# Performance work log

Hardware: AMD Instinct MI355X
Metric: run time of the kernel (lower is better)

## Reference

```python
import jax, jax.numpy as jnp
import numpy as np

HIDDEN = 1024
HEADS = 16
HEAD_DIM = HIDDEN // HEADS
B, S = 2, 2048


def setup_inputs() -> dict:
    key = jax.random.key(0)
    k1, k2, k3 = jax.random.split(key, 3)
    scale_in = 1.0 / np.sqrt(HIDDEN)
    x = jax.random.normal(k1, (B, S, HIDDEN), dtype=jnp.float32)
    wqkv_w = jax.random.normal(k2, (3 * HIDDEN, HIDDEN), dtype=jnp.float32) * scale_in
    wo_w = jax.random.normal(k3, (HIDDEN, HIDDEN), dtype=jnp.float32) * scale_in
    wo_b = jnp.zeros((HIDDEN,), dtype=jnp.float32)
    return {"x": x, "wqkv_w": wqkv_w, "wo_w": wo_w, "wo_b": wo_b}


def reference(x, wqkv_w, wo_w, wo_b):
    b, s, d = x.shape
    h, hd = HEADS, HEAD_DIM
    sm_scale = hd ** (-0.5)
    # QKV projection (torch Linear: x @ W^T), then chunk into q,k,v
    qkv = jnp.einsum('bsd,ed->bse', x, wqkv_w)  # [b, s, 3d]
    q, k, v = jnp.split(qkv, 3, axis=-1)
    # [b, h, s, hd]
    q = q.reshape(b, s, h, hd).transpose(0, 2, 1, 3)
    k = k.reshape(b, s, h, hd).transpose(0, 2, 1, 3)
    v = v.reshape(b, s, h, hd).transpose(0, 2, 1, 3)
    # raw scores, then causal mask (mask applied BEFORE scaling, as in source;
    # -inf * scale == -inf so math matches softmax(score*scale) with mask)
    scores = jnp.einsum('bhqe,bhke->bhqk', q, k)
    causal = jnp.tril(jnp.ones((s, s), dtype=bool))
    scores = jnp.where(causal[None, None, :, :], scores, -jnp.inf)
    weights = jax.nn.softmax(scores * sm_scale, axis=-1)
    # dropout p=0.0 (eval) -> identity
    out = jnp.einsum('bhqk,bhke->bhqe', weights, v)
    out = out.transpose(0, 2, 1, 3).reshape(b, s, h * hd)
    y = jnp.einsum('bsd,ed->bse', out, wo_w) + wo_b
    return (y, k, v)
```

## Files before the change

kernel.cpp:

```cpp
#include <hip/hip_runtime.h>
#include <cstdint>
#include <cstddef>


using bf16x8 = __attribute__((ext_vector_type(8))) __bf16;
using f32x4  = __attribute__((ext_vector_type(4))) float;
using u16    = unsigned short;

#define SOFT_SCALE 0.1803368801111244f

__device__ __forceinline__ u16 f2bf(float f) {
  union { float f; uint32_t u; } a; a.f = f;
  uint32_t r = a.u + 0x7fffu + ((a.u >> 16) & 1u);
  return (u16)(r >> 16);
}

__device__ __forceinline__ bf16x8 ldfrag(const u16* p) {
  return *reinterpret_cast<const bf16x8*>(p);
}

__device__ __forceinline__ void gload_lds16(const void* g, void* l) {
  __builtin_amdgcn_global_load_lds((const __attribute__((address_space(1))) void*)g,
                                   (__attribute__((address_space(3))) void*)l,
                                   16, 0, 0);
}

__device__ __forceinline__ uint32_t cvt_pk_bf16(float a, float b) {
  uint32_t r;
  asm("v_cvt_pk_bf16_f32 %0, %1, %2" : "=v"(r) : "v"(a), "v"(b));
  return r;
}

__global__ void cvt_all(const float* __restrict__ x, const float* __restrict__ wqkv,
                        const float* __restrict__ wo,
                        u16* __restrict__ xb, u16* __restrict__ wqkvb, u16* __restrict__ wob) {
  int i = blockIdx.x * blockDim.x + threadIdx.x;
  int stride = gridDim.x * blockDim.x;
  for (; i < 2097152; i += stride) {
    const float* src; u16* dst; int j;
    if (i < 1048576)      { src = x;    dst = xb;    j = i; }
    else if (i < 1835008) { src = wqkv; dst = wqkvb; j = i - 1048576; }
    else                  { src = wo;   dst = wob;   j = i - 1835008; }
    float4 v = reinterpret_cast<const float4*>(src)[j];
    ushort4 o;
    o.x = f2bf(v.x); o.y = f2bf(v.y); o.z = f2bf(v.z); o.w = f2bf(v.w);
    reinterpret_cast<ushort4*>(dst)[j] = o;
  }
}

__global__ __launch_bounds__(512, 2) void qkv_gemm_kernel(
    const u16* __restrict__ Xb, const u16* __restrict__ Wb,
    u16* __restrict__ Qws, u16* __restrict__ Kws, u16* __restrict__ Vtws,
    float* __restrict__ out) {
  extern __shared__ char smem[];

  const int tid = threadIdx.x, lane = tid & 63, wid = tid >> 6;
  const int wr = wid >> 2, wc = wid & 3;
  const int fq = lane >> 4, fr = lane & 15;

  const int wg = (blockIdx.x & 7) * 24 + (blockIdx.x >> 3);
  const int bm = wg / 12, bn = wg % 12;
  const int m0 = bm * 256, n0 = bn * 256;

  const char* Ab = (const char*)Xb + (size_t)m0 * 2048;
  const char* Bb = (const char*)Wb + (size_t)n0 * 2048;

  f32x4 acc[8][4] = {};

  auto stage = [&](int t, int cc) {
    char* As = smem + cc * 32768;
    char* Bs = smem + 65536 + cc * 32768;
#pragma unroll
    for (int f = 0; f < 4; ++f) {
      int lin = (f * 512 + tid) * 16;
      int row = lin >> 7;
      int col = (lin & 127) ^ ((row & 7) << 4);
      gload_lds16(Ab + (size_t)row * 2048 + t * 128 + col, As + lin);
      gload_lds16(Bb + (size_t)row * 2048 + t * 128 + col, Bs + lin);
    }
  };

  stage(0, 0);
  int cur = 0;
  for (int t = 0; t < 16; ++t) {
    if (t < 15) {
      stage(t + 1, cur ^ 1);
      asm volatile("s_waitcnt vmcnt(8)" ::: "memory");
    } else {
      asm volatile("s_waitcnt vmcnt(0)" ::: "memory");
    }
    __builtin_amdgcn_s_barrier();
    __builtin_amdgcn_sched_barrier(0);

    const char* As = smem + cur * 32768;
    const char* Bs = smem + 65536 + cur * 32768;

#pragma unroll
    for (int ks = 0; ks < 2; ++ks) {
      bf16x8 af[8];
#pragma unroll
      for (int m = 0; m < 8; ++m) {
        int row = wr * 128 + m * 16 + fr;
        int col = (ks * 64 + fq * 16) ^ ((row & 7) << 4);
        af[m] = *(const bf16x8*)(As + row * 128 + col);
      }
#pragma unroll
      for (int nh = 0; nh < 2; ++nh) {
        int row0 = wc * 64 + (nh * 2) * 16 + fr;
        int col0 = (ks * 64 + fq * 16) ^ ((row0 & 7) << 4);
        bf16x8 bf0 = *(const bf16x8*)(Bs + row0 * 128 + col0);
        int row1 = wc * 64 + (nh * 2 + 1) * 16 + fr;
        int col1 = (ks * 64 + fq * 16) ^ ((row1 & 7) << 4);
        bf16x8 bf1 = *(const bf16x8*)(Bs + row1 * 128 + col1);
        __builtin_amdgcn_s_setprio(1);
#pragma unroll
        for (int m = 0; m < 8; ++m) {
          acc[m][nh * 2]     = __builtin_amdgcn_mfma_f32_16x16x32_bf16(af[m], bf0, acc[m][nh * 2], 0, 0, 0);
          acc[m][nh * 2 + 1] = __builtin_amdgcn_mfma_f32_16x16x32_bf16(af[m], bf1, acc[m][nh * 2 + 1], 0, 0, 0);
        }
        __builtin_amdgcn_s_setprio(0);
      }
    }
    asm volatile("s_waitcnt lgkmcnt(0)" ::: "memory");
    __builtin_amdgcn_s_barrier();
    cur ^= 1;
  }

  const int sect = n0 >> 10;
  const int nn0 = (n0 & 1023) + wc * 64;
  const int mbase = m0 + wr * 128;
#pragma unroll
  for (int m = 0; m < 8; ++m)
#pragma unroll
    for (int n = 0; n < 4; ++n) {
      int mB = mbase + m * 16 + fq * 4;
      int ncol = nn0 + n * 16 + fr;
      int b = mB >> 11, s0 = mB & 2047;
      int h = ncol >> 6, hd = ncol & 63;
      size_t base = (((size_t)b * 16 + h) * 2048 + s0) * 64 + hd;
      float v0 = acc[m][n][0], v1 = acc[m][n][1], v2 = acc[m][n][2], v3 = acc[m][n][3];
      if (sect == 0) {
        Qws[base]       = f2bf(v0 * SOFT_SCALE);
        Qws[base + 64]  = f2bf(v1 * SOFT_SCALE);
        Qws[base + 128] = f2bf(v2 * SOFT_SCALE);
        Qws[base + 192] = f2bf(v3 * SOFT_SCALE);
      } else if (sect == 1) {
        Kws[base] = f2bf(v0); Kws[base + 64] = f2bf(v1);
        Kws[base + 128] = f2bf(v2); Kws[base + 192] = f2bf(v3);
        out[4194304 + base] = v0; out[4194304 + base + 64] = v1;
        out[4194304 + base + 128] = v2; out[4194304 + base + 192] = v3;
      } else {
        out[8388608 + base] = v0; out[8388608 + base + 64] = v1;
        out[8388608 + base + 128] = v2; out[8388608 + base + 192] = v3;
        size_t tt = ((size_t)(b * 16 + h) * 64 + hd) * 2048 + s0;
        ushort4 pk; pk.x = f2bf(v0); pk.y = f2bf(v1); pk.z = f2bf(v2); pk.w = f2bf(v3);
        *reinterpret_cast<ushort4*>(Vtws + tt) = pk;
      }
    }
}

__device__ __forceinline__ void gemm128_core(const u16* __restrict__ A,
                                             const u16* __restrict__ B,
                                             int m0, int n0, int K,
                                             u16* As, u16* Bs, f32x4 acc[4][4]) {
  const int tid  = threadIdx.x;
  const int lane = tid & 63;
  const int wid  = tid >> 6;
  const int wr = wid >> 1, wc = wid & 1;
  const int fq = lane >> 4, fr = lane & 15;

  for (int kb = 0; kb < K; kb += 32) {
#pragma unroll
    for (int j = 0; j < 2; ++j) {
      int lin = (j * 256 + tid) * 16;
      int row = lin >> 6;
      int rb  = lin & 63;
      gload_lds16((const char*)(A + (size_t)(m0 + row) * K + kb) + rb, (char*)As + lin);
      gload_lds16((const char*)(B + (size_t)(n0 + row) * K + kb) + rb, (char*)Bs + lin);
    }
    __syncthreads();

    bf16x8 av[4], bv[4];
#pragma unroll
    for (int i = 0; i < 4; ++i) av[i] = ldfrag(As + (wr * 64 + i * 16 + fr) * 32 + fq * 8);
#pragma unroll
    for (int j = 0; j < 4; ++j) bv[j] = ldfrag(Bs + (wc * 64 + j * 16 + fr) * 32 + fq * 8);
    __builtin_amdgcn_s_setprio(1);
#pragma unroll
    for (int i = 0; i < 4; ++i)
#pragma unroll
      for (int j = 0; j < 4; ++j)
        acc[i][j] = __builtin_amdgcn_mfma_f32_16x16x32_bf16(av[i], bv[j], acc[i][j], 0, 0, 0);
    __builtin_amdgcn_s_setprio(0);
    __syncthreads();
  }
}

__global__ __launch_bounds__(256, 4) void attn_kernel(
    const u16* __restrict__ Qw, const u16* __restrict__ Kw,
    const u16* __restrict__ Vtw, u16* __restrict__ Ow) {
  __shared__ u16 Ks[2][64 * 64];
  __shared__ u16 Vs[2][64 * 64];

  const int tid = threadIdx.x, lane = tid & 63, wid = tid >> 6;
  const int fq = lane >> 4, fr = lane & 15;
  const int bh = blockIdx.x & 31;
  const int qb = 31 - (blockIdx.x >> 5);
  const int b = bh >> 4, h = bh & 15;
  const int q0 = qb * 64;

  const u16* Qbase  = Qw  + (size_t)bh * 2048 * 64;
  const u16* Kbase  = Kw  + (size_t)bh * 2048 * 64;
  const char* VtBase = (const char*)(Vtw + (size_t)bh * 64 * 2048);

#pragma unroll
  for (int f = 0; f < 2; ++f) {
    int lin = (f * 256 + tid) * 16;
    int row = lin >> 7;
    int logical = lin ^ ((row & 7) << 4);
    gload_lds16((const char*)Kbase + logical, (char*)Ks[0] + lin);
    gload_lds16(VtBase + (size_t)row * 4096 + (logical & 127), (char*)Vs[0] + lin);
  }

  const int qrow = q0 + wid * 16 + fr;
  bf16x8 qa0 = ldfrag(Qbase + (size_t)qrow * 64 + fq * 8);
  bf16x8 qa1 = ldfrag(Qbase + (size_t)qrow * 64 + 32 + fq * 8);

  float ssum = 0.f;
  f32x4 accO[4] = {};

  int cur = 0;
  for (int kb = 0; kb <= qb; ++kb) {
    __syncthreads();

    if (kb < qb) {
      const char* kg = (const char*)(Kbase + (size_t)(kb + 1) * 64 * 64);
#pragma unroll
      for (int f = 0; f < 2; ++f) {
        int lin = (f * 256 + tid) * 16;
        int row = lin >> 7;
        int logical = lin ^ ((row & 7) << 4);
        gload_lds16(kg + logical, (char*)Ks[cur ^ 1] + lin);
        gload_lds16(VtBase + (size_t)row * 4096 + (size_t)(kb + 1) * 128 + (logical & 127),
                    (char*)Vs[cur ^ 1] + lin);
      }
    }

    const u16* Kc = Ks[cur];
    const u16* Vc = Vs[cur];

    f32x4 sfr[4];
    __builtin_amdgcn_s_setprio(1);
#pragma unroll
    for (int n = 0; n < 4; ++n) {
      int krow = n * 16 + fr;
      bf16x8 kf0 = ldfrag(Kc + krow * 64 + ((fq * 8)      ^ ((krow & 7) << 3)));
      bf16x8 kf1 = ldfrag(Kc + krow * 64 + ((fq * 8 + 32) ^ ((krow & 7) << 3)));
      f32x4 z = {};
      z = __builtin_amdgcn_mfma_f32_16x16x32_bf16(kf0, qa0, z, 0, 0, 0);
      z = __builtin_amdgcn_mfma_f32_16x16x32_bf16(kf1, qa1, z, 0, 0, 0);
      sfr[n] = z;
    }
    __builtin_amdgcn_s_setprio(0);

    uint32_t W[4][2];
#pragma unroll
    for (int n = 0; n < 4; ++n) {
      float p0, p1, p2, p3;
      if (kb < qb) {
        p0 = exp2f(sfr[n][0]);
        p1 = exp2f(sfr[n][1]);
        p2 = exp2f(sfr[n][2]);
        p3 = exp2f(sfr[n][3]);
      } else {
        int kvg = kb * 64 + n * 16 + fq * 4;
        p0 = (kvg + 0 > qrow) ? 0.f : exp2f(sfr[n][0]);
        p1 = (kvg + 1 > qrow) ? 0.f : exp2f(sfr[n][1]);
        p2 = (kvg + 2 > qrow) ? 0.f : exp2f(sfr[n][2]);
        p3 = (kvg + 3 > qrow) ? 0.f : exp2f(sfr[n][3]);
      }
      ssum += (p0 + p1) + (p2 + p3);
      W[n][0] = cvt_pk_bf16(p0, p1);
      W[n][1] = cvt_pk_bf16(p2, p3);
    }

    union { uint32_t u[4]; bf16x8 v; } pa0u, pa1u;
#pragma unroll
    for (int hh = 0; hh < 2; ++hh) {
      uint32_t a0 = W[0][hh], b0 = W[1][hh];
      asm("v_permlane32_swap_b32 %0, %1" : "+v"(a0), "+v"(b0));
      asm("v_permlane16_swap_b32 %0, %1" : "+v"(a0), "+v"(b0));
      pa0u.u[hh] = a0; pa0u.u[2 + hh] = b0;
      uint32_t a1 = W[2][hh], b1 = W[3][hh];
      asm("v_permlane32_swap_b32 %0, %1" : "+v"(a1), "+v"(b1));
      asm("v_permlane16_swap_b32 %0, %1" : "+v"(a1), "+v"(b1));
      pa1u.u[hh] = a1; pa1u.u[2 + hh] = b1;
    }

    __builtin_amdgcn_s_setprio(1);
#pragma unroll
    for (int nh = 0; nh < 4; ++nh) {
      int vrow = nh * 16 + fr;
      bf16x8 vb0 = ldfrag(Vc + vrow * 64 + ((fq * 8)      ^ ((vrow & 7) << 3)));
      bf16x8 vb1 = ldfrag(Vc + vrow * 64 + ((fq * 8 + 32) ^ ((vrow & 7) << 3)));
      accO[nh] = __builtin_amdgcn_mfma_f32_16x16x32_bf16(pa0u.v, vb0, accO[nh], 0, 0, 0);
      accO[nh] = __builtin_amdgcn_mfma_f32_16x16x32_bf16(pa1u.v, vb1, accO[nh], 0, 0, 0);
    }
    __builtin_amdgcn_s_setprio(0);
    cur ^= 1;
  }

  ssum += __shfl_xor(ssum, 16);
  ssum += __shfl_xor(ssum, 32);
  float inv = 1.0f / ssum;
  float invq[4];
#pragma unroll
  for (int r = 0; r < 4; ++r) invq[r] = __shfl(inv, fq * 4 + r);

#pragma unroll
  for (int nh = 0; nh < 4; ++nh)
#pragma unroll
    for (int r = 0; r < 4; ++r) {
      float o = accO[nh][r] * invq[r];
      int qr = q0 + wid * 16 + fq * 4 + r;
      Ow[((size_t)b * 2048 + qr) * 1024 + h * 64 + nh * 16 + fr] = f2bf(o);
    }
}

__global__ __launch_bounds__(256) void proj_gemm_kernel(
    const u16* __restrict__ Ob, const u16* __restrict__ Wob,
    const float* __restrict__ bias, float* __restrict__ out) {
  __shared__ u16 As[128 * 32];
  __shared__ u16 Bs[128 * 32];
  const int NB = 8;
  int m0 = (blockIdx.x / NB) * 128, n0 = (blockIdx.x % NB) * 128;
  f32x4 acc[4][4] = {};
  gemm128_core(Ob, Wob, m0, n0, 1024, As, Bs, acc);

  const int lane = threadIdx.x & 63, wid = threadIdx.x >> 6;
  const int wr = wid >> 1, wc = wid & 1, fq = lane >> 4, fr = lane & 15;
#pragma unroll
  for (int i = 0; i < 4; ++i)
#pragma unroll
    for (int j = 0; j < 4; ++j)
#pragma unroll
      for (int r = 0; r < 4; ++r) {
        int m = m0 + wr * 64 + i * 16 + fq * 4 + r;
        int n = n0 + wc * 64 + j * 16 + fr;
        out[(size_t)m * 1024 + n] = acc[i][j][r] + bias[n];
      }
}

extern "C" void kernel_launch(void* const* d_in, const int* in_sizes, int n_in,
                              void* d_out, int out_size, void* d_ws, size_t ws_size,
                              hipStream_t stream) {
  const float* x    = (const float*)d_in[0];
  const float* wqkv = (const float*)d_in[1];
  const float* wo   = (const float*)d_in[2];
  const float* wo_b = (const float*)d_in[3];
  float* out = (float*)d_out;

  u16* xb    = (u16*)d_ws;
  u16* wqkvb = xb    + 4194304;
  u16* wob   = wqkvb + 3145728;
  u16* q_ws  = wob   + 1048576;
  u16* k_ws  = q_ws  + 4194304;
  u16* vt_ws = k_ws  + 4194304;
  u16* o_ws  = vt_ws + 4194304;

  static bool attr_set = false;
  if (!attr_set) {
    hipFuncSetAttribute((const void*)qkv_gemm_kernel,
                        hipFuncAttributeMaxDynamicSharedMemorySize, 131072);
    attr_set = true;
  }

  cvt_all<<<2048, 256, 0, stream>>>(x, wqkv, wo, xb, wqkvb, wob);
  qkv_gemm_kernel<<<192, 512, 131072, stream>>>(xb, wqkvb, q_ws, k_ws, vt_ws, out);
  attn_kernel<<<32 * 32, 256, 0, stream>>>(q_ws, k_ws, vt_ws, o_ws);
  proj_gemm_kernel<<<32 * 8, 256, 0, stream>>>(o_ws, wob, wo_b, out);
}
```

Baseline: 119.1 us.

## Split long causal attention rows across two blocks and add a combine kernel

Query blocks in the upper half of the causal range now split their key range into two halves, each handled by its own block. Each half writes unnormalized bf16 partial outputs and row sums into reused workspace, and a new combine kernel adds them and normalizes. This shortens the critical path set by the longest causal rows and balances work across CUs. The cost is an extra kernel launch, extra partial-result traffic, and bf16 rounding of unnormalized partial sums.

```diff
diff --git a/kernel.cpp b/kernel.cpp
--- a/kernel.cpp
+++ b/kernel.cpp
@@ -13,6 +13,11 @@
   union { float f; uint32_t u; } a; a.f = f;
   uint32_t r = a.u + 0x7fffu + ((a.u >> 16) & 1u);
   return (u16)(r >> 16);
+}
+
+__device__ __forceinline__ float bf2f(u16 u) {
+  union { uint32_t u; float f; } a; a.u = ((uint32_t)u) << 16;
+  return a.f;
 }
 
 __device__ __forceinline__ bf16x8 ldfrag(const u16* p) {
@@ -198,14 +203,21 @@
 
 __global__ __launch_bounds__(256, 4) void attn_kernel(
     const u16* __restrict__ Qw, const u16* __restrict__ Kw,
-    const u16* __restrict__ Vtw, u16* __restrict__ Ow) {
+    const u16* __restrict__ Vtw, u16* __restrict__ Ow,
+    u16* __restrict__ Pb, float* __restrict__ Sb) {
   __shared__ u16 Ks[2][64 * 64];
   __shared__ u16 Vs[2][64 * 64];
 
   const int tid = threadIdx.x, lane = tid & 63, wid = tid >> 6;
   const int fq = lane >> 4, fr = lane & 15;
   const int bh = blockIdx.x & 31;
-  const int qb = 31 - (blockIdx.x >> 5);
+  const int j  = blockIdx.x >> 5;
+  int qb, sp, nsplit;
+  if (j < 32) { qb = 31 - (j >> 1); sp = j & 1; nsplit = 2; }
+  else        { qb = 47 - j;        sp = 0;     nsplit = 1; }
+  const int len = (qb + 2) >> 1;
+  const int lo  = (nsplit == 2) ? sp * len : 0;
+  const int hi  = (nsplit == 2) ? min(lo + len, qb + 1) : qb + 1;
   const int b = bh >> 4, h = bh & 15;
   const int q0 = qb * 64;
 
@@ -213,14 +225,19 @@
   const u16* Kbase  = Kw  + (size_t)bh * 2048 * 64;
   const char* VtBase = (const char*)(Vtw + (size_t)bh * 64 * 2048);
 
-#pragma unroll
-  for (int f = 0; f < 2; ++f) {
-    int lin = (f * 256 + tid) * 16;
-    int row = lin >> 7;
-    int logical = lin ^ ((row & 7) << 4);
-    gload_lds16((const char*)Kbase + logical, (char*)Ks[0] + lin);
-    gload_lds16(VtBase + (size_t)row * 4096 + (logical & 127), (char*)Vs[0] + lin);
-  }
+  auto stageKV = [&](int kt, int cc) {
+#pragma unroll
+    for (int f = 0; f < 2; ++f) {
+      int lin = (f * 256 + tid) * 16;
+      int row = lin >> 7;
+      int logical = lin ^ ((row & 7) << 4);
+      gload_lds16((const char*)Kbase + (size_t)kt * 8192 + logical, (char*)Ks[cc] + lin);
+      gload_lds16(VtBase + (size_t)row * 4096 + (size_t)kt * 128 + (logical & 127),
+                  (char*)Vs[cc] + lin);
+    }
+  };
+
+  stageKV(lo, 0);
 
   const int qrow = q0 + wid * 16 + fr;
   bf16x8 qa0 = ldfrag(Qbase + (size_t)qrow * 64 + fq * 8);
@@ -230,21 +247,10 @@
   f32x4 accO[4] = {};
 
   int cur = 0;
-  for (int kb = 0; kb <= qb; ++kb) {
+  for (int kb = lo; kb < hi; ++kb) {
     __syncthreads();
 
-    if (kb < qb) {
-      const char* kg = (const char*)(Kbase + (size_t)(kb + 1) * 64 * 64);
-#pragma unroll
-      for (int f = 0; f < 2; ++f) {
-        int lin = (f * 256 + tid) * 16;
-        int row = lin >> 7;
-        int logical = lin ^ ((row & 7) << 4);
-        gload_lds16(kg + logical, (char*)Ks[cur ^ 1] + lin);
-        gload_lds16(VtBase + (size_t)row * 4096 + (size_t)(kb + 1) * 128 + (logical & 127),
-                    (char*)Vs[cur ^ 1] + lin);
-      }
-    }
+    if (kb + 1 < hi) stageKV(kb + 1, cur ^ 1);
 
     const u16* Kc = Ks[cur];
     const u16* Vc = Vs[cur];
@@ -312,19 +318,62 @@
 
   ssum += __shfl_xor(ssum, 16);
   ssum += __shfl_xor(ssum, 32);
-  float inv = 1.0f / ssum;
-  float invq[4];
-#pragma unroll
-  for (int r = 0; r < 4; ++r) invq[r] = __shfl(inv, fq * 4 + r);
-
-#pragma unroll
-  for (int nh = 0; nh < 4; ++nh)
-#pragma unroll
-    for (int r = 0; r < 4; ++r) {
-      float o = accO[nh][r] * invq[r];
-      int qr = q0 + wid * 16 + fq * 4 + r;
-      Ow[((size_t)b * 2048 + qr) * 1024 + h * 64 + nh * 16 + fr] = f2bf(o);
-    }
+
+  if (nsplit == 1) {
+    float inv = 1.0f / ssum;
+    float invq[4];
+#pragma unroll
+    for (int r = 0; r < 4; ++r) invq[r] = __shfl(inv, fq * 4 + r);
+#pragma unroll
+    for (int nh = 0; nh < 4; ++nh)
+#pragma unroll
+      for (int r = 0; r < 4; ++r) {
+        float o = accO[nh][r] * invq[r];
+        int qr = q0 + wid * 16 + fq * 4 + r;
+        Ow[((size_t)b * 2048 + qr) * 1024 + h * 64 + nh * 16 + fr] = f2bf(o);
+      }
+  } else {
+    int slot = ((bh * 16 + (qb - 16)) << 1) + sp;
+    u16* po = Pb + (size_t)slot * 4096;
+    if (fq == 0) Sb[slot * 64 + wid * 16 + fr] = ssum;
+#pragma unroll
+    for (int nh = 0; nh < 4; ++nh)
+#pragma unroll
+      for (int r = 0; r < 4; ++r) {
+        int ql = wid * 16 + fq * 4 + r;
+        po[ql * 64 + nh * 16 + fr] = f2bf(accO[nh][r]);
+      }
+  }
+}
+
+__global__ __launch_bounds__(256) void attn_combine(
+    const u16* __restrict__ Pb, const float* __restrict__ Sb,
+    u16* __restrict__ Ow) {
+  int idx = blockIdx.x;
+  int bh = idx >> 4, qq = idx & 15;
+  int qb = 16 + qq;
+  int slot = (bh * 16 + qq) << 1;
+  const u16* p0 = Pb + (size_t)slot * 4096;
+  const float* s0 = Sb + slot * 64;
+  int t = threadIdx.x;
+  int q = t >> 2, c0 = (t & 3) * 16;
+  float inv = 1.0f / (s0[q] + s0[64 + q]);
+  int b = bh >> 4, h = bh & 15;
+  int qr = qb * 64 + q;
+  size_t obase = ((size_t)b * 2048 + qr) * 1024 + h * 64 + c0;
+
+  union { uint4 v[2]; u16 e[16]; } a, bb, o;
+  a.v[0]  = *(const uint4*)(p0 + q * 64 + c0);
+  a.v[1]  = *(const uint4*)(p0 + q * 64 + c0 + 8);
+  bb.v[0] = *(const uint4*)(p0 + 4096 + q * 64 + c0);
+  bb.v[1] = *(const uint4*)(p0 + 4096 + q * 64 + c0 + 8);
+#pragma unroll
+  for (int e = 0; e < 16; ++e) {
+    float v = bf2f(a.e[e]) + bf2f(bb.e[e]);
+    o.e[e] = f2bf(v * inv);
+  }
+  *(uint4*)(Ow + obase)     = o.v[0];
+  *(uint4*)(Ow + obase + 8) = o.v[1];
 }
 
 __global__ __launch_bounds__(256) void proj_gemm_kernel(
@@ -368,6 +417,9 @@
   u16* vt_ws = k_ws  + 4194304;
   u16* o_ws  = vt_ws + 4194304;
 
+  u16*   part_o = xb;
+  float* part_s = (float*)wqkvb;
+
   static bool attr_set = false;
   if (!attr_set) {
     hipFuncSetAttribute((const void*)qkv_gemm_kernel,
@@ -377,6 +429,7 @@
 
   cvt_all<<<2048, 256, 0, stream>>>(x, wqkv, wo, xb, wqkvb, wob);
   qkv_gemm_kernel<<<192, 512, 131072, stream>>>(xb, wqkvb, q_ws, k_ws, vt_ws, out);
-  attn_kernel<<<32 * 32, 256, 0, stream>>>(q_ws, k_ws, vt_ws, o_ws);
+  attn_kernel<<<48 * 32, 256, 0, stream>>>(q_ws, k_ws, vt_ws, o_ws, part_o, part_s);
+  attn_combine<<<512, 256, 0, stream>>>(part_o, part_s, o_ws);
   proj_gemm_kernel<<<32 * 8, 256, 0, stream>>>(o_ws, wob, wo_b, out);
 }
```

After: 123.7 us. 3.8% more time.

## Restructure QKV GEMM main loop into four-phase half-tile pipelined schedule

Applied to the files above, without the earlier changes.

Splits each K-step of the QKV projection GEMM into four compute phases over half-tiles of A and B. Global-to-LDS loads of half tiles are interleaved between MFMA phases, with B prefetched two steps ahead. Fragment reads are narrowed to fit the phases. The aim is finer-grained overlap of memory and matrix work, in the style of HipKittens 8-wave ping-pong. The cost is many more barriers and a tricky vmcnt accounting that could race or stall.

```diff
diff --git a/kernel.cpp b/kernel.cpp
--- a/kernel.cpp
+++ b/kernel.cpp
@@ -67,63 +67,120 @@
 
   f32x4 acc[8][4] = {};
 
-  auto stage = [&](int t, int cc) {
-    char* As = smem + cc * 32768;
-    char* Bs = smem + 65536 + cc * 32768;
-#pragma unroll
-    for (int f = 0; f < 4; ++f) {
-      int lin = (f * 512 + tid) * 16;
-      int row = lin >> 7;
-      int col = (lin & 127) ^ ((row & 7) << 4);
-      gload_lds16(Ab + (size_t)row * 2048 + t * 128 + col, As + lin);
-      gload_lds16(Bb + (size_t)row * 2048 + t * 128 + col, Bs + lin);
+  auto stage_half = [&](int t, int mat, int h) {
+    char* dst = smem + mat * 65536 + (t & 1) * 32768 + h * 16384;
+    const char* src = mat ? Bb : Ab;
+#pragma unroll
+    for (int l = 0; l < 2; ++l) {
+      int lin = (l * 512 + tid) * 16;
+      int rl  = lin >> 7;
+      int col = (lin & 127) ^ ((rl & 7) << 4);
+      gload_lds16(src + (size_t)(h * 128 + rl) * 2048 + t * 128 + col, dst + lin);
     }
   };
 
-  stage(0, 0);
-  int cur = 0;
+  stage_half(0, 0, 0); stage_half(0, 0, 1);
+  stage_half(0, 1, 0); stage_half(0, 1, 1);
+  stage_half(1, 1, 0); stage_half(1, 1, 1);
+  asm volatile("s_waitcnt vmcnt(4)" ::: "memory");
+  __builtin_amdgcn_s_barrier();
+
+  bf16x8 afr[4][2];
+  bf16x8 bfr[4][2];
+
   for (int t = 0; t < 16; ++t) {
+    const char* As = smem + (t & 1) * 32768;
+    const char* Bs = smem + 65536 + (t & 1) * 32768;
+
+#pragma unroll
+    for (int m = 0; m < 4; ++m) {
+      int row = wr * 128 + m * 16 + fr;
+#pragma unroll
+      for (int ks = 0; ks < 2; ++ks)
+        afr[m][ks] = *(const bf16x8*)(As + row * 128 + ((ks * 64 + fq * 16) ^ ((row & 7) << 4)));
+    }
+#pragma unroll
+    for (int n = 0; n < 2; ++n) {
+      int row = wc * 64 + n * 16 + fr;
+#pragma unroll
+      for (int ks = 0; ks < 2; ++ks)
+        bfr[n][ks] = *(const bf16x8*)(Bs + row * 128 + ((ks * 64 + fq * 16) ^ ((row & 7) << 4)));
+    }
+    if (t + 1 < 16) stage_half(t + 1, 0, 0);
+    __builtin_amdgcn_s_barrier();
+    asm volatile("s_waitcnt lgkmcnt(0)" ::: "memory");
+    __builtin_amdgcn_sched_barrier(0);
+    __builtin_amdgcn_s_setprio(1);
+#pragma unroll
+    for (int m = 0; m < 4; ++m)
+#pragma unroll
+      for (int n = 0; n < 2; ++n)
+#pragma unroll
+        for (int ks = 0; ks < 2; ++ks)
+          acc[m][n] = __builtin_amdgcn_mfma_f32_16x16x32_bf16(afr[m][ks], bfr[n][ks], acc[m][n], 0, 0, 0);
+    __builtin_amdgcn_s_setprio(0);
+    __builtin_amdgcn_s_barrier();
+
+#pragma unroll
+    for (int n = 2; n < 4; ++n) {
+      int row = wc * 64 + n * 16 + fr;
+#pragma unroll
+      for (int ks = 0; ks < 2; ++ks)
+        bfr[n][ks] = *(const bf16x8*)(Bs + row * 128 + ((ks * 64 + fq * 16) ^ ((row & 7) << 4)));
+    }
+    if (t + 1 < 16) stage_half(t + 1, 0, 1);
+    __builtin_amdgcn_s_barrier();
+    asm volatile("s_waitcnt lgkmcnt(0)" ::: "memory");
+    __builtin_amdgcn_sched_barrier(0);
+    __builtin_amdgcn_s_setprio(1);
+#pragma unroll
+    for (int m = 0; m < 4; ++m)
+#pragma unroll
+      for (int n = 2; n < 4; ++n)
+#pragma unroll
+        for (int ks = 0; ks < 2; ++ks)
+          acc[m][n] = __builtin_amdgcn_mfma_f32_16x16x32_bf16(afr[m][ks], bfr[n][ks], acc[m][n], 0, 0, 0);
+    __builtin_amdgcn_s_setprio(0);
+    __builtin_amdgcn_s_barrier();
+
+#pragma unroll
+    for (int m = 0; m < 4; ++m) {
+      int row = wr * 128 + (m + 4) * 16 + fr;
+#pragma unroll
+      for (int ks = 0; ks < 2; ++ks)
+        afr[m][ks] = *(const bf16x8*)(As + row * 128 + ((ks * 64 + fq * 16) ^ ((row & 7) << 4)));
+    }
+    if (t + 2 < 16) stage_half(t + 2, 1, 0);
+    __builtin_amdgcn_s_barrier();
+    asm volatile("s_waitcnt lgkmcnt(0)" ::: "memory");
+    __builtin_amdgcn_sched_barrier(0);
+    __builtin_amdgcn_s_setprio(1);
+#pragma unroll
+    for (int m = 0; m < 4; ++m)
+#pragma unroll
+      for (int n = 0; n < 2; ++n)
+#pragma unroll
+        for (int ks = 0; ks < 2; ++ks)
+          acc[m + 4][n] = __builtin_amdgcn_mfma_f32_16x16x32_bf16(afr[m][ks], bfr[n][ks], acc[m + 4][n], 0, 0, 0);
+    __builtin_amdgcn_s_setprio(0);
+    __builtin_amdgcn_s_barrier();
+
+    if (t + 2 < 16) stage_half(t + 2, 1, 1);
+    __builtin_amdgcn_s_barrier();
+    __builtin_amdgcn_s_setprio(1);
+#pragma unroll
+    for (int m = 0; m < 4; ++m)
+#pragma unroll
+      for (int n = 2; n < 4; ++n)
+#pragma unroll
+        for (int ks = 0; ks < 2; ++ks)
+          acc[m + 4][n] = __builtin_amdgcn_mfma_f32_16x16x32_bf16(afr[m][ks], bfr[n][ks], acc[m + 4][n], 0, 0, 0);
+    __builtin_amdgcn_s_setprio(0);
     if (t < 15) {
-      stage(t + 1, cur ^ 1);
-      asm volatile("s_waitcnt vmcnt(8)" ::: "memory");
-    } else {
-      asm volatile("s_waitcnt vmcnt(0)" ::: "memory");
-    }
-    __builtin_amdgcn_s_barrier();
-    __builtin_amdgcn_sched_barrier(0);
-
-    const char* As = smem + cur * 32768;
-    const char* Bs = smem + 65536 + cur * 32768;
-
-#pragma unroll
-    for (int ks = 0; ks < 2; ++ks) {
-      bf16x8 af[8];
-#pragma unroll
-      for (int m = 0; m < 8; ++m) {
-        int row = wr * 128 + m * 16 + fr;
-        int col = (ks * 64 + fq * 16) ^ ((row & 7) << 4);
-        af[m] = *(const bf16x8*)(As + row * 128 + col);
-      }
-#pragma unroll
-      for (int nh = 0; nh < 2; ++nh) {
-        int row0 = wc * 64 + (nh * 2) * 16 + fr;
-        int col0 = (ks * 64 + fq * 16) ^ ((row0 & 7) << 4);
-        bf16x8 bf0 = *(const bf16x8*)(Bs + row0 * 128 + col0);
-        int row1 = wc * 64 + (nh * 2 + 1) * 16 + fr;
-        int col1 = (ks * 64 + fq * 16) ^ ((row1 & 7) << 4);
-        bf16x8 bf1 = *(const bf16x8*)(Bs + row1 * 128 + col1);
-        __builtin_amdgcn_s_setprio(1);
-#pragma unroll
-        for (int m = 0; m < 8; ++m) {
-          acc[m][nh * 2]     = __builtin_amdgcn_mfma_f32_16x16x32_bf16(af[m], bf0, acc[m][nh * 2], 0, 0, 0);
-          acc[m][nh * 2 + 1] = __builtin_amdgcn_mfma_f32_16x16x32_bf16(af[m], bf1, acc[m][nh * 2 + 1], 0, 0, 0);
-        }
-        __builtin_amdgcn_s_setprio(0);
-      }
-    }
-    asm volatile("s_waitcnt lgkmcnt(0)" ::: "memory");
-    __builtin_amdgcn_s_barrier();
-    cur ^= 1;
+      if (t == 14) asm volatile("s_waitcnt vmcnt(0)" ::: "memory");
+      else         asm volatile("s_waitcnt vmcnt(4)" ::: "memory");
+    }
+    __builtin_amdgcn_s_barrier();
   }
 
   const int sect = n0 >> 10;
```

Measured after the change: 117.8 us. About the same (-1.1%).
